# Performance work log

Hardware: AMD Instinct MI355X
Metric: run time of the kernel (lower is better)

## Reference

```python
import jax, jax.numpy as jnp
import numpy as np

H = 1024
NH = 16
B = 32
S = 4096


def setup_inputs() -> dict:
    key = jax.random.key(0)
    ks = jax.random.split(key, 9)
    std = 0.02
    return {
        "x": jax.random.normal(ks[0], (B, S, H), dtype=jnp.float32),
        "Wq": jax.random.normal(ks[1], (H, H), dtype=jnp.float32) * std,
        "bq": jax.random.normal(ks[2], (H,), dtype=jnp.float32) * std,
        "Wk": jax.random.normal(ks[3], (H, H), dtype=jnp.float32) * std,
        "bk": jax.random.normal(ks[4], (H,), dtype=jnp.float32) * std,
        "Wv": jax.random.normal(ks[5], (H, H), dtype=jnp.float32) * std,
        "bv": jax.random.normal(ks[6], (H,), dtype=jnp.float32) * std,
        "Wo": jax.random.normal(ks[7], (H, H), dtype=jnp.float32) * std,
        "bo": jax.random.normal(ks[8], (H,), dtype=jnp.float32) * std,
        "n_heads": NH,
    }


def reference(x, Wq, bq, Wk, bk, Wv, bv, Wo, bo, n_heads):
    b, s, h = x.shape
    dk = h // n_heads
    scale = dk ** -0.5
    # Q only from last position (decode-style single query)
    q = (x[:, -1, :] @ Wq.T + bq).reshape(b, n_heads, dk)          # (B,H,dk)
    k = (x @ Wk.T + bk).reshape(b, s, n_heads, dk)                 # (B,S,H,dk)
    v = (x @ Wv.T + bv).reshape(b, s, n_heads, dk)
    scores = jnp.einsum('bhd,bshd->bhs', q, k) * scale             # (B,H,S)
    attn = jax.nn.softmax(scores, axis=-1)
    out = jnp.einsum('bhs,bshd->bhd', attn, v).reshape(b, h)       # (B,hidden)
    return out @ Wo.T + bo
```

## Files before the change

### kernel.cpp

```cpp
#include <hip/hip_runtime.h>
#include <hip/hip_bf16.h>

#define B_  32
#define S_  4096
#define H_  1024
#define NH_ 16
#define DK_ 64
#define NCH 32
#define ROWS 128
#define TILE 4
#define NT (ROWS / TILE)

#define Q_OFF  0
#define T_OFF  (Q_OFF + B_*H_)
#define YP_OFF (T_OFF + B_*NH_*H_)
#define ML_OFF (YP_OFF + NCH*B_*NH_*H_)
#define Y2_OFF (ML_OFF + NCH*B_*2*NH_)
#define OP_OFF (Y2_OFF + B_*NH_*H_)

#define DOT4(a, v) ((a).x*(v).x + (a).y*(v).y + (a).z*(v).z + (a).w*(v).w)

template <int CTRL>
__device__ __forceinline__ float dppadd(float v) {
  int mv = __builtin_amdgcn_update_dpp(0, __float_as_int(v), CTRL, 0xF, 0xF, true);
  return v + __int_as_float(mv);
}

__global__ __launch_bounds__(256) void k_q(const float* __restrict__ x,
                                           const float* __restrict__ Wq,
                                           const float* __restrict__ bq,
                                           float* __restrict__ q) {
  __shared__ __align__(16) float xl[4 * H_];
  int islab = blockIdx.x, bg = blockIdx.y, tid = threadIdx.x;
  #pragma unroll
  for (int k = 0; k < 4; ++k) {
    int idx4 = k * 256 + tid;
    int bl = idx4 >> 8, col4 = idx4 & 255;
    *(float4*)&xl[bl * H_ + col4 * 4] =
        *(const float4*)(x + (((size_t)(bg * 4 + bl)) * S_ + (S_ - 1)) * H_ + col4 * 4);
  }
  __syncthreads();
  int d = tid >> 2, p = tid & 3;
  int i = islab * 64 + d;
  const float* w = Wq + (size_t)i * H_ + p * 256;
  float acc[4] = {0.f, 0.f, 0.f, 0.f};
  #pragma unroll 4
  for (int jj = 0; jj < 256; jj += 4) {
    float4 wv = *(const float4*)(w + jj);
    #pragma unroll
    for (int bl = 0; bl < 4; ++bl) {
      float4 xv = *(const float4*)&xl[bl * H_ + p * 256 + jj];
      acc[bl] += DOT4(xv, wv);
    }
  }
  #pragma unroll
  for (int bl = 0; bl < 4; ++bl) {
    acc[bl] += __shfl_xor(acc[bl], 1);
    acc[bl] += __shfl_xor(acc[bl], 2);
  }
  if (p == 0) {
    float bias = bq[i];
    #pragma unroll
    for (int bl = 0; bl < 4; ++bl)
      q[(size_t)(bg * 4 + bl) * H_ + i] = acc[bl] + bias;
  }
}

__global__ __launch_bounds__(256) void k_t(const float* __restrict__ q,
                                           const float* __restrict__ Wk,
                                           float* __restrict__ t) {
  __shared__ __align__(16) float qh[B_ * DK_];
  int js = blockIdx.x, h = blockIdx.y, tid = threadIdx.x;
  #pragma unroll
  for (int k = 0; k < 2; ++k) {
    int idx4 = k * 256 + tid;
    int bl = idx4 >> 4, d4 = idx4 & 15;
    *(float4*)&qh[bl * DK_ + d4 * 4] =
        *(const float4*)(q + (size_t)bl * H_ + h * DK_ + d4 * 4);
  }
  __syncthreads();

  int bh = tid >> 7;
  int j = js * 128 + (tid & 127);
  float acc[16];
  #pragma unroll
  for (int bl = 0; bl < 16; ++bl) acc[bl] = 0.f;
  for (int d = 0; d < DK_; ++d) {
    float wv = Wk[((size_t)(h * DK_ + d)) * H_ + j];
    #pragma unroll
    for (int bl = 0; bl < 16; ++bl) acc[bl] += qh[(bh * 16 + bl) * DK_ + d] * wv;
  }
  #pragma unroll
  for (int bl = 0; bl < 16; ++bl)
    t[((size_t)((bh * 16 + bl) * NH_ + h)) * H_ + j] = acc[bl];
}

__global__ __launch_bounds__(256) void k_flash(const float* __restrict__ x,
                                               const float* __restrict__ t,
                                               float* __restrict__ ypart,
                                               float* __restrict__ mlpart) {
  int ch = blockIdx.x, b = blockIdx.y, tid = threadIdx.x;
  int wv = tid >> 6, ln = tid & 63;

  const float* xg = x + ((size_t)b * S_ + (size_t)ch * ROWS) * H_ + ln * 16;

  float4 tf[4][4];
  #pragma unroll
  for (int hh = 0; hh < 4; ++hh) {
    const float* tg = t + ((size_t)b * NH_ + wv * 4 + hh) * H_ + ln * 16;
    #pragma unroll
    for (int j = 0; j < 4; ++j) tf[hh][j] = *(const float4*)(tg + j * 4);
  }

  float4 ya[4][4];
  #pragma unroll
  for (int hh = 0; hh < 4; ++hh)
    #pragma unroll
    for (int j = 0; j < 4; ++j) {
      ya[hh][j].x = 0.f; ya[hh][j].y = 0.f; ya[hh][j].z = 0.f; ya[hh][j].w = 0.f;
    }
  float m_r[4] = {-3.4e38f, -3.4e38f, -3.4e38f, -3.4e38f};
  float l_r[4] = {0.f, 0.f, 0.f, 0.f};

  #pragma unroll 1
  for (int u = 0; u < NT; ++u) {
    float4 xr[TILE][4];
    #pragma unroll
    for (int s = 0; s < TILE; ++s) {
      const float* xrow = xg + (size_t)(u * TILE + s) * H_;
      #pragma unroll
      for (int j = 0; j < 4; ++j) xr[s][j] = *(const float4*)(xrow + j * 4);
    }

    float scr[4][TILE];
    #pragma unroll
    for (int hh = 0; hh < 4; ++hh)
      #pragma unroll
      for (int s = 0; s < TILE; ++s) {
        float a = DOT4(xr[s][0], tf[hh][0]);
        a += DOT4(xr[s][1], tf[hh][1]);
        a += DOT4(xr[s][2], tf[hh][2]);
        a += DOT4(xr[s][3], tf[hh][3]);
        scr[hh][s] = a;
      }

    #pragma unroll
    for (int hh = 0; hh < 4; ++hh)
      #pragma unroll
      for (int s = 0; s < TILE; ++s) {
        float a = scr[hh][s];
        a = dppadd<0xB1>(a);
        a = dppadd<0x4E>(a);
        a = dppadd<0x141>(a);
        a = dppadd<0x140>(a);
        a += __shfl_xor(a, 16);
        a += __shfl_xor(a, 32);
        scr[hh][s] = a * 0.125f;
      }

    #pragma unroll
    for (int hh = 0; hh < 4; ++hh) {
      float tmax = fmaxf(fmaxf(scr[hh][0], scr[hh][1]), fmaxf(scr[hh][2], scr[hh][3]));
      float mnew = fmaxf(m_r[hh], tmax);
      float fac = __expf(m_r[hh] - mnew);
      float e0 = __expf(scr[hh][0] - mnew);
      float e1 = __expf(scr[hh][1] - mnew);
      float e2 = __expf(scr[hh][2] - mnew);
      float e3 = __expf(scr[hh][3] - mnew);
      m_r[hh] = mnew;
      l_r[hh] = l_r[hh] * fac + (e0 + e1 + e2 + e3);
      #pragma unroll
      for (int j = 0; j < 4; ++j) {
        float4 y0 = ya[hh][j];
        y0.x = y0.x * fac + e0 * xr[0][j].x + e1 * xr[1][j].x + e2 * xr[2][j].x + e3 * xr[3][j].x;
        y0.y = y0.y * fac + e0 * xr[0][j].y + e1 * xr[1][j].y + e2 * xr[2][j].y + e3 * xr[3][j].y;
        y0.z = y0.z * fac + e0 * xr[0][j].z + e1 * xr[1][j].z + e2 * xr[2][j].z + e3 * xr[3][j].z;
        y0.w = y0.w * fac + e0 * xr[0][j].w + e1 * xr[1][j].w + e2 * xr[2][j].w + e3 * xr[3][j].w;
        ya[hh][j] = y0;
      }
    }
  }

  float* yo = ypart + ((size_t)(ch * B_ + b)) * NH_ * H_ + ln * 16;
  #pragma unroll
  for (int hh = 0; hh < 4; ++hh)
    #pragma unroll
    for (int j = 0; j < 4; ++j)
      *(float4*)(yo + (size_t)(wv * 4 + hh) * H_ + j * 4) = ya[hh][j];
  if (ln == 0) {
    #pragma unroll
    for (int hh = 0; hh < 4; ++hh) {
      size_t base = ((size_t)(ch * B_ + b)) * (2 * NH_) + (size_t)(wv * 4 + hh) * 2;
      mlpart[base + 0] = m_r[hh];
      mlpart[base + 1] = l_r[hh];
    }
  }
}

__global__ __launch_bounds__(256) void k_yred(const float* __restrict__ ypart,
                                              const float* __restrict__ mlpart,
                                              float* __restrict__ y2) {
  int h = blockIdx.x, b = blockIdx.y, tid = threadIdx.x;
  float mg = -3.4e38f;
  for (int ch = 0; ch < NCH; ++ch)
    mg = fmaxf(mg, mlpart[((size_t)(ch * B_ + b)) * (2 * NH_) + h * 2]);
  float L = 0.f;
  float4 acc; acc.x = acc.y = acc.z = acc.w = 0.f;
  for (int ch = 0; ch < NCH; ++ch) {
    float mc = mlpart[((size_t)(ch * B_ + b)) * (2 * NH_) + h * 2 + 0];
    float lc = mlpart[((size_t)(ch * B_ + b)) * (2 * NH_) + h * 2 + 1];
    float w = __expf(mc - mg);
    L += w * lc;
    float4 v = *(const float4*)(ypart +
        ((size_t)(ch * B_ + b)) * NH_ * H_ + (size_t)h * H_ + tid * 4);
    acc.x += w * v.x; acc.y += w * v.y; acc.z += w * v.z; acc.w += w * v.w;
  }
  float inv = 1.f / L;
  acc.x *= inv; acc.y *= inv; acc.z *= inv; acc.w *= inv;
  *(float4*)(y2 + ((size_t)(b * NH_ + h)) * H_ + tid * 4) = acc;
}

__global__ __launch_bounds__(256) void k_vproj(const float* __restrict__ y2,
                                               const float* __restrict__ Wv,
                                               const float* __restrict__ bv,
                                               float* __restrict__ op) {
  __shared__ __align__(16) float yl[4 * H_];
  int h = blockIdx.x, bg = blockIdx.y, tid = threadIdx.x;
  #pragma unroll
  for (int k = 0; k < 4; ++k) {
    int idx4 = k * 256 + tid;
    int bl = idx4 >> 8, col4 = idx4 & 255;
    *(float4*)&yl[bl * H_ + col4 * 4] =
        *(const float4*)(y2 + ((size_t)((bg * 4 + bl) * NH_ + h)) * H_ + col4 * 4);
  }
  __syncthreads();
  int d = tid >> 2, p = tid & 3;
  const float* w = Wv + ((size_t)(h * DK_ + d)) * H_ + p * 256;
  float acc[4] = {0.f, 0.f, 0.f, 0.f};
  #pragma unroll 4
  for (int jj = 0; jj < 256; jj += 4) {
    float4 wv = *(const float4*)(w + jj);
    #pragma unroll
    for (int bl = 0; bl < 4; ++bl) {
      float4 yv = *(const float4*)&yl[bl * H_ + p * 256 + jj];
      acc[bl] += DOT4(yv, wv);
    }
  }
  #pragma unroll
  for (int bl = 0; bl < 4; ++bl) {
    acc[bl] += __shfl_xor(acc[bl], 1);
    acc[bl] += __shfl_xor(acc[bl], 2);
  }
  if (p == 0) {
    float bias = bv[h * DK_ + d];
    #pragma unroll
    for (int bl = 0; bl < 4; ++bl)
      op[(size_t)(bg * 4 + bl) * H_ + h * DK_ + d] = acc[bl] + bias;
  }
}

__global__ __launch_bounds__(256) void k_out(const float* __restrict__ op,
                                             const float* __restrict__ Wo,
                                             const float* __restrict__ bo,
                                             float* __restrict__ out) {
  __shared__ __align__(16) float ul[4 * H_];
  int islab = blockIdx.x, bg = blockIdx.y, tid = threadIdx.x;
  #pragma unroll
  for (int k = 0; k < 4; ++k) {
    int idx4 = k * 256 + tid;
    int bl = idx4 >> 8, col4 = idx4 & 255;
    *(float4*)&ul[bl * H_ + col4 * 4] =
        *(const float4*)(op + (size_t)(bg * 4 + bl) * H_ + col4 * 4);
  }
  __syncthreads();
  int d = tid >> 2, p = tid & 3;
  int i = islab * 64 + d;
  const float* w = Wo + (size_t)i * H_ + p * 256;
  float acc[4] = {0.f, 0.f, 0.f, 0.f};
  #pragma unroll 4
  for (int jj = 0; jj < 256; jj += 4) {
    float4 wv = *(const float4*)(w + jj);
    #pragma unroll
    for (int bl = 0; bl < 4; ++bl) {
      float4 uv = *(const float4*)&ul[bl * H_ + p * 256 + jj];
      acc[bl] += DOT4(uv, wv);
    }
  }
  #pragma unroll
  for (int bl = 0; bl < 4; ++bl) {
    acc[bl] += __shfl_xor(acc[bl], 1);
    acc[bl] += __shfl_xor(acc[bl], 2);
  }
  if (p == 0) {
    float bias = bo[i];
    #pragma unroll
    for (int bl = 0; bl < 4; ++bl)
      out[(size_t)(bg * 4 + bl) * H_ + i] = acc[bl] + bias;
  }
}

extern "C" void kernel_launch(void* const* d_in, const int* in_sizes, int n_in,
                              void* d_out, int out_size, void* d_ws, size_t ws_size,
                              hipStream_t stream) {
  const float* x  = (const float*)d_in[0];
  const float* Wq = (const float*)d_in[1];
  const float* bq = (const float*)d_in[2];
  const float* Wk = (const float*)d_in[3];
  const float* Wv = (const float*)d_in[5];
  const float* bv = (const float*)d_in[6];
  const float* Wo = (const float*)d_in[7];
  const float* bo = (const float*)d_in[8];
  float* out = (float*)d_out;
  float* ws = (float*)d_ws;

  float* q  = ws + Q_OFF;
  float* t  = ws + T_OFF;
  float* yp = ws + YP_OFF;
  float* ml = ws + ML_OFF;
  float* y2 = ws + Y2_OFF;
  float* op = ws + OP_OFF;

  k_q<<<dim3(16, B_ / 4), 256, 0, stream>>>(x, Wq, bq, q);
  k_t<<<dim3(8, NH_), 256, 0, stream>>>(q, Wk, t);
  k_flash<<<dim3(NCH, B_), 256, 0, stream>>>(x, t, yp, ml);
  k_yred<<<dim3(NH_, B_), 256, 0, stream>>>(yp, ml, y2);
  k_vproj<<<dim3(NH_, B_ / 4), 256, 0, stream>>>(y2, Wv, bv, op);
  k_out<<<dim3(16, B_ / 4), 256, 0, stream>>>(op, Wo, bo, out);
}
```

Measured before the change: 287.2 us.

## Double-buffer x tiles in flash kernel and split heads across eight waves

The flash-decode kernel now runs 512 threads per block, with each wave handling 2 heads instead of 4. Chunks are twice as long, so there are half as many partial results to reduce. The row loop is software-pipelined with two register buffers, so the next x tile is loaded while the current one is being processed. This is meant to hide global-load latency and cut per-wave register pressure. In exchange, each x row is now read by eight waves instead of four, which adds cache traffic, and the grid has fewer blocks. The last iteration also issues one redundant prefetch.

After: 419.8 us. 1.46x slower.

```diff
diff --git a/kernel.cpp b/kernel.cpp
--- a/kernel.cpp
+++ b/kernel.cpp
@@ -6,8 +6,8 @@
 #define H_  1024
 #define NH_ 16
 #define DK_ 64
-#define NCH 32
-#define ROWS 128
+#define NCH 16
+#define ROWS 256
 #define TILE 4
 #define NT (ROWS / TILE)
 
@@ -95,7 +95,7 @@
     t[((size_t)((bh * 16 + bl) * NH_ + h)) * H_ + j] = acc[bl];
 }
 
-__global__ __launch_bounds__(256) void k_flash(const float* __restrict__ x,
+__global__ __launch_bounds__(512) void k_flash(const float* __restrict__ x,
                                                const float* __restrict__ t,
                                                float* __restrict__ ypart,
                                                float* __restrict__ mlpart) {
@@ -104,93 +104,105 @@
 
   const float* xg = x + ((size_t)b * S_ + (size_t)ch * ROWS) * H_ + ln * 16;
 
-  float4 tf[4][4];
-  #pragma unroll
-  for (int hh = 0; hh < 4; ++hh) {
-    const float* tg = t + ((size_t)b * NH_ + wv * 4 + hh) * H_ + ln * 16;
+  float4 tf[2][4];
+  #pragma unroll
+  for (int hh = 0; hh < 2; ++hh) {
+    const float* tg = t + ((size_t)b * NH_ + wv * 2 + hh) * H_ + ln * 16;
     #pragma unroll
     for (int j = 0; j < 4; ++j) tf[hh][j] = *(const float4*)(tg + j * 4);
   }
 
-  float4 ya[4][4];
-  #pragma unroll
-  for (int hh = 0; hh < 4; ++hh)
+  float4 ya[2][4];
+  #pragma unroll
+  for (int hh = 0; hh < 2; ++hh)
     #pragma unroll
     for (int j = 0; j < 4; ++j) {
       ya[hh][j].x = 0.f; ya[hh][j].y = 0.f; ya[hh][j].z = 0.f; ya[hh][j].w = 0.f;
     }
-  float m_r[4] = {-3.4e38f, -3.4e38f, -3.4e38f, -3.4e38f};
-  float l_r[4] = {0.f, 0.f, 0.f, 0.f};
-
+  float m_r[2] = {-3.4e38f, -3.4e38f};
+  float l_r[2] = {0.f, 0.f};
+
+  float4 xa[TILE][4], xb[TILE][4];
+
+#define LOADX(dst, tl)                                                        \
+  {                                                                           \
+    _Pragma("unroll") for (int s_ = 0; s_ < TILE; ++s_) {                     \
+      const float* xrow_ = xg + (size_t)((tl) * TILE + s_) * H_;              \
+      _Pragma("unroll") for (int j_ = 0; j_ < 4; ++j_)                        \
+          dst[s_][j_] = *(const float4*)(xrow_ + j_ * 4);                     \
+    }                                                                         \
+  }
+
+#define COMPUTE(src)                                                          \
+  {                                                                           \
+    float scr[2][TILE];                                                       \
+    _Pragma("unroll") for (int hh = 0; hh < 2; ++hh)                          \
+      _Pragma("unroll") for (int s = 0; s < TILE; ++s) {                      \
+        float a = DOT4(src[s][0], tf[hh][0]);                                 \
+        a += DOT4(src[s][1], tf[hh][1]);                                      \
+        a += DOT4(src[s][2], tf[hh][2]);                                      \
+        a += DOT4(src[s][3], tf[hh][3]);                                      \
+        scr[hh][s] = a;                                                       \
+      }                                                                       \
+    _Pragma("unroll") for (int hh = 0; hh < 2; ++hh)                          \
+      _Pragma("unroll") for (int s = 0; s < TILE; ++s) {                      \
+        float a = scr[hh][s];                                                 \
+        a = dppadd<0xB1>(a);                                                  \
+        a = dppadd<0x4E>(a);                                                  \
+        a = dppadd<0x141>(a);                                                 \
+        a = dppadd<0x140>(a);                                                 \
+        a += __shfl_xor(a, 16);                                               \
+        a += __shfl_xor(a, 32);                                               \
+        scr[hh][s] = a * 0.125f;                                              \
+      }                                                                       \
+    _Pragma("unroll") for (int hh = 0; hh < 2; ++hh) {                        \
+      float tmax = fmaxf(fmaxf(scr[hh][0], scr[hh][1]),                       \
+                         fmaxf(scr[hh][2], scr[hh][3]));                      \
+      float mnew = fmaxf(m_r[hh], tmax);                                      \
+      float fac = __expf(m_r[hh] - mnew);                                     \
+      float e0 = __expf(scr[hh][0] - mnew);                                   \
+      float e1 = __expf(scr[hh][1] - mnew);                                   \
+      float e2 = __expf(scr[hh][2] - mnew);                                   \
+      float e3 = __expf(scr[hh][3] - mnew);                                   \
+      m_r[hh] = mnew;                                                         \
+      l_r[hh] = l_r[hh] * fac + (e0 + e1 + e2 + e3);                          \
+      _Pragma("unroll") for (int j = 0; j < 4; ++j) {                         \
+        float4 y0 = ya[hh][j];                                                \
+        y0.x = y0.x * fac + e0 * src[0][j].x + e1 * src[1][j].x               \
+                          + e2 * src[2][j].x + e3 * src[3][j].x;              \
+        y0.y = y0.y * fac + e0 * src[0][j].y + e1 * src[1][j].y               \
+                          + e2 * src[2][j].y + e3 * src[3][j].y;              \
+        y0.z = y0.z * fac + e0 * src[0][j].z + e1 * src[1][j].z               \
+                          + e2 * src[2][j].z + e3 * src[3][j].z;              \
+        y0.w = y0.w * fac + e0 * src[0][j].w + e1 * src[1][j].w               \
+                          + e2 * src[2][j].w + e3 * src[3][j].w;              \
+        ya[hh][j] = y0;                                                       \
+      }                                                                       \
+    }                                                                         \
+  }
+
+  LOADX(xa, 0);
   #pragma unroll 1
-  for (int u = 0; u < NT; ++u) {
-    float4 xr[TILE][4];
-    #pragma unroll
-    for (int s = 0; s < TILE; ++s) {
-      const float* xrow = xg + (size_t)(u * TILE + s) * H_;
-      #pragma unroll
-      for (int j = 0; j < 4; ++j) xr[s][j] = *(const float4*)(xrow + j * 4);
-    }
-
-    float scr[4][TILE];
-    #pragma unroll
-    for (int hh = 0; hh < 4; ++hh)
-      #pragma unroll
-      for (int s = 0; s < TILE; ++s) {
-        float a = DOT4(xr[s][0], tf[hh][0]);
-        a += DOT4(xr[s][1], tf[hh][1]);
-        a += DOT4(xr[s][2], tf[hh][2]);
-        a += DOT4(xr[s][3], tf[hh][3]);
-        scr[hh][s] = a;
-      }
-
-    #pragma unroll
-    for (int hh = 0; hh < 4; ++hh)
-      #pragma unroll
-      for (int s = 0; s < TILE; ++s) {
-        float a = scr[hh][s];
-        a = dppadd<0xB1>(a);
-        a = dppadd<0x4E>(a);
-        a = dppadd<0x141>(a);
-        a = dppadd<0x140>(a);
-        a += __shfl_xor(a, 16);
-        a += __shfl_xor(a, 32);
-        scr[hh][s] = a * 0.125f;
-      }
-
-    #pragma unroll
-    for (int hh = 0; hh < 4; ++hh) {
-      float tmax = fmaxf(fmaxf(scr[hh][0], scr[hh][1]), fmaxf(scr[hh][2], scr[hh][3]));
-      float mnew = fmaxf(m_r[hh], tmax);
-      float fac = __expf(m_r[hh] - mnew);
-      float e0 = __expf(scr[hh][0] - mnew);
-      float e1 = __expf(scr[hh][1] - mnew);
-      float e2 = __expf(scr[hh][2] - mnew);
-      float e3 = __expf(scr[hh][3] - mnew);
-      m_r[hh] = mnew;
-      l_r[hh] = l_r[hh] * fac + (e0 + e1 + e2 + e3);
-      #pragma unroll
-      for (int j = 0; j < 4; ++j) {
-        float4 y0 = ya[hh][j];
-        y0.x = y0.x * fac + e0 * xr[0][j].x + e1 * xr[1][j].x + e2 * xr[2][j].x + e3 * xr[3][j].x;
-        y0.y = y0.y * fac + e0 * xr[0][j].y + e1 * xr[1][j].y + e2 * xr[2][j].y + e3 * xr[3][j].y;
-        y0.z = y0.z * fac + e0 * xr[0][j].z + e1 * xr[1][j].z + e2 * xr[2][j].z + e3 * xr[3][j].z;
-        y0.w = y0.w * fac + e0 * xr[0][j].w + e1 * xr[1][j].w + e2 * xr[2][j].w + e3 * xr[3][j].w;
-        ya[hh][j] = y0;
-      }
-    }
-  }
+  for (int u = 0; u < NT; u += 2) {
+    LOADX(xb, u + 1);
+    COMPUTE(xa);
+    int t2 = (u + 2 < NT) ? u + 2 : 0;
+    LOADX(xa, t2);
+    COMPUTE(xb);
+  }
+#undef LOADX
+#undef COMPUTE
 
   float* yo = ypart + ((size_t)(ch * B_ + b)) * NH_ * H_ + ln * 16;
   #pragma unroll
-  for (int hh = 0; hh < 4; ++hh)
+  for (int hh = 0; hh < 2; ++hh)
     #pragma unroll
     for (int j = 0; j < 4; ++j)
-      *(float4*)(yo + (size_t)(wv * 4 + hh) * H_ + j * 4) = ya[hh][j];
+      *(float4*)(yo + (size_t)(wv * 2 + hh) * H_ + j * 4) = ya[hh][j];
   if (ln == 0) {
     #pragma unroll
-    for (int hh = 0; hh < 4; ++hh) {
-      size_t base = ((size_t)(ch * B_ + b)) * (2 * NH_) + (size_t)(wv * 4 + hh) * 2;
+    for (int hh = 0; hh < 2; ++hh) {
+      size_t base = ((size_t)(ch * B_ + b)) * (2 * NH_) + (size_t)(wv * 2 + hh) * 2;
       mlpart[base + 0] = m_r[hh];
       mlpart[base + 1] = l_r[hh];
     }
@@ -322,7 +334,7 @@
 
   k_q<<<dim3(16, B_ / 4), 256, 0, stream>>>(x, Wq, bq, q);
   k_t<<<dim3(8, NH_), 256, 0, stream>>>(q, Wk, t);
-  k_flash<<<dim3(NCH, B_), 256, 0, stream>>>(x, t, yp, ml);
+  k_flash<<<dim3(NCH, B_), 512, 0, stream>>>(x, t, yp, ml);
   k_yred<<<dim3(NH_, B_), 256, 0, stream>>>(yp, ml, y2);
   k_vproj<<<dim3(NH_, B_ / 4), 256, 0, stream>>>(y2, Wv, bv, op);
   k_out<<<dim3(16, B_ / 4), 256, 0, stream>>>(op, Wo, bo, out);
```
